# Kernel tuning notes

Measured on AMD Instinct MI355X. Metric: run time of the kernel, lower is better.

Reference implementation:

```python
import jax, jax.numpy as jnp
import numpy as np

NUM_BASES = 8
DEGREE = 3
KSIZE = 3
DOMAIN = (0.0, 1.0)


def bspline_basis(x, degree, knots):
    """Cox-de Boor recursion, vectorized over all elements of x.
    x: [...] float; knots: [num_bases + degree + 1].
    Returns basis values of shape [..., num_bases].
    (The original torch code evaluates this same recursion per-tap inside
    nested loops; here it is evaluated once, batched, with correct knot
    index bookkeeping. Uniform distinct knots -> no zero denominators.)
    """
    xe = x[..., None]  # [..., 1]
    # degree-0: indicator of each knot interval -> [..., L-1]
    B = ((knots[:-1] <= xe) & (xe < knots[1:])).astype(x.dtype)
    for d in range(1, degree + 1):
        left = (xe - knots[:-(d + 1)]) / (knots[d:-1] - knots[:-(d + 1)]) * B[..., :-1]
        right = (knots[d + 1:] - xe) / (knots[d + 1:] - knots[1:-d]) * B[..., 1:]
        B = left + right  # [..., L-d-1]
    return B  # [..., num_bases]


def setup_inputs() -> dict:
    key = jax.random.key(0)
    k1, k2 = jax.random.split(key)
    # inputs uniform in [0,1) so they lie inside the B-spline domain
    x = jax.random.uniform(k1, (16, 64, 64, 64), dtype=jnp.float32)
    # per-tap spline coefficients: [Cout, Cin, K, K, num_bases]
    coeff = jax.random.normal(k2, (64, 64, KSIZE, KSIZE, NUM_BASES), dtype=jnp.float32)
    return {"x": x, "coeff": coeff}


def reference(x, coeff):
    # normalize to domain (identity for domain=(0,1), kept for faithfulness)
    xn = (x - DOMAIN[0]) / (DOMAIN[1] - DOMAIN[0])
    knots = jnp.linspace(DOMAIN[0], DOMAIN[1], NUM_BASES + DEGREE + 1, dtype=x.dtype)
    # spline basis for every input element: [B, Cin, H, W, nb]
    phi = bspline_basis(xn, DEGREE, knots)
    Bn, Cin, H, W, nb = phi.shape
    Cout = coeff.shape[0]
    # The KAN conv  out[b,o,h,w] = sum_{j,k,l,m} phi[b,j,h+k,w+l,m]*coeff[o,j,k,l,m]
    # is exactly a VALID conv with Cin*nb input channels.
    phi_c = jnp.transpose(phi, (0, 1, 4, 2, 3)).reshape(Bn, Cin * nb, H, W)
    w = jnp.transpose(coeff, (0, 1, 4, 2, 3)).reshape(Cout, Cin * nb, KSIZE, KSIZE)
    out = jax.lax.conv_general_dilated(
        phi_c, w, window_strides=(1, 1), padding="VALID",
        dimension_numbers=("NCHW", "OIHW", "NCHW"))
    return out  # [B, Cout, H-K+1, W-K+1]
```

## Files before the change

kernel.cpp:

```cpp
#include <hip/hip_runtime.h>
#include <hip/hip_bf16.h>


typedef short v8s __attribute__((ext_vector_type(8)));
typedef float v4f __attribute__((ext_vector_type(4)));
typedef float v16f __attribute__((ext_vector_type(16)));
typedef unsigned long long u64;
typedef u64 v2u64 __attribute__((ext_vector_type(2)));

#define B_N   16
#define CIN   64
#define COUT  64
#define H_IN  64
#define W_IN  64
#define NB    8
#define HO    62
#define WO    62
#define JC    8
#define NCH   8

__device__ __forceinline__ ushort f2bf(float f) {
    uint xu = __float_as_uint(f);
    return (ushort)((xu + 0x7fffu + ((xu >> 16) & 1u)) >> 16);
}

__device__ __forceinline__ uint cvtpk(float a, float b) {
    uint r;
    asm("v_cvt_pk_bf16_f32 %0, %1, %2" : "=v"(r) : "v"(a), "v"(b));
    return r;
}

__global__ void prep_coeff_kernel(const float* __restrict__ coeff, ushort* __restrict__ bt) {
    int n = blockIdx.x * 256 + threadIdx.x;
    if (n >= 294912) return;
    int m  = n & 7;
    int g2 = (n >> 3) & 1;
    int o  = (n >> 4) & 63;
    int jp = (n >> 10) & 3;
    int q  = n >> 12;
    int tap = q % 9;
    int jc  = q / 9;
    int j = jc * 8 + jp * 2 + g2;
    bt[n] = f2bf(coeff[((o * CIN + j) * 9 + tap) * 8 + m]);
}

#define MFMA32(a, b, c) __builtin_amdgcn_mfma_f32_32x32x16_bf16((a), (b), (c), 0, 0, 0)
#define MFMA16(a, b, c) __builtin_amdgcn_mfma_f32_16x16x32_bf16((a), (b), (c), 0, 0, 0)

__global__ __launch_bounds__(512, 4) void kan_conv_hp2(
        const float* __restrict__ x, const ushort* __restrict__ cb,
        float* __restrict__ out) {
    extern __shared__ __align__(16) char smraw[];
    const int h0   = blockIdx.x * 2;
    const int b    = blockIdx.y;
    const int tid  = threadIdx.x;
    const int lane = tid & 63;
    const int wv   = tid >> 6;
    const int kh   = wv & 3;
    const int hh   = wv >> 2;
    const int l31  = lane & 31;
    const int g2   = lane >> 5;

    char* wrB = smraw + wv * 6144 + lane * 16;
    const char* rdB = smraw + wv * 6144 + g2 * 1024 + l31 * 16;

    v16f acc[2][2];
    acc[0][0] = (v16f)(0.f); acc[0][1] = (v16f)(0.f);
    acc[1][0] = (v16f)(0.f); acc[1][1] = (v16f)(0.f);

    float xr0[6], xr1[6];
    const float* xb = x + ((size_t)(b * CIN) * H_IN + (h0 + hh)) * W_IN + lane;
    const int jx = kh * 2;

#define XL(dst, jcn) { \
    _Pragma("unroll") \
    for (int e = 0; e < 6; ++e) \
        dst[e] = xb[(size_t)((jcn) * 8 + jx + (e & 1)) * (H_IN * W_IN) + (e >> 1) * W_IN]; \
    }

    auto PW = [&](float xval, int e) {
        float s_ = fminf(fmaxf(xval * 11.0f, 0.0f), 10.999f);
        int i0 = (int)s_;
        float u  = s_ - (float)i0;
        float um = 1.0f - u;
        float u2 = u * u, u3 = u2 * u;
        const float inv6 = 1.0f / 6.0f;
        float n0 = um * um * um * inv6;
        float n1 = (3.0f * u3 - 6.0f * u2 + 4.0f) * inv6;
        float n2 = (-3.0f * u3 + 3.0f * u2 + 3.0f * u + 1.0f) * inv6;
        float n3 = u3 * inv6;
        u64 V = (u64)cvtpk(n0, n1) | ((u64)cvtpk(n2, n3) << 32);
        int bi = i0 - 3;
        u64 lo = bi < 0 ? (V >> (uint)(-16 * bi))
               : bi < 4 ? (V << (uint)(16 * bi)) : 0ull;
        u64 hi = bi <= 0 ? 0ull
               : bi < 4 ? (V >> (uint)(64 - 16 * bi))
               : (V << (uint)(16 * bi - 64));
        v2u64 pk; pk[0] = lo; pk[1] = hi;
        *reinterpret_cast<v2u64*>(wrB + e * 1024) = pk;
    };
    auto TAP = [&](const char* pAc, int k, int lt, int tap) {
        v8s b0 = *reinterpret_cast<const v8s*>(rdB + k * 2048 + lt * 16);
        v8s b1 = *reinterpret_cast<const v8s*>(rdB + k * 2048 + 512 + lt * 16);
        v8s a0 = *reinterpret_cast<const v8s*>(pAc + tap * 8192);
        v8s a1 = *reinterpret_cast<const v8s*>(pAc + tap * 8192 + 1024);
        acc[0][0] = MFMA32(a0, b0, acc[0][0]);
        acc[0][1] = MFMA32(a0, b1, acc[0][1]);
        acc[1][0] = MFMA32(a1, b0, acc[1][0]);
        acc[1][1] = MFMA32(a1, b1, acc[1][1]);
    };

    const char* pA = (const char*)cb + (size_t)(kh * 128 + l31 * 2 + g2) * 16;

    XL(xr0, 0);
    PW(xr0[0], 0); PW(xr0[1], 1); PW(xr0[2], 2);
    PW(xr0[3], 3); PW(xr0[4], 4); PW(xr0[5], 5);
    XL(xr1, 1);

#define CHUNK(jc, CUR, NXT) { \
    const char* pAc = pA + (size_t)(jc) * 73728; \
    if ((jc) + 2 < NCH) XL(NXT, (jc) + 2); \
    TAP(pAc, 0, 0, 0); TAP(pAc, 0, 1, 1); TAP(pAc, 0, 2, 2); \
    if ((jc) + 1 < NCH) { PW(CUR[0], 0); PW(CUR[1], 1); } \
    TAP(pAc, 1, 0, 3); TAP(pAc, 1, 1, 4); TAP(pAc, 1, 2, 5); \
    if ((jc) + 1 < NCH) { PW(CUR[2], 2); PW(CUR[3], 3); } \
    TAP(pAc, 2, 0, 6); TAP(pAc, 2, 1, 7); TAP(pAc, 2, 2, 8); \
    if ((jc) + 1 < NCH) { PW(CUR[4], 4); PW(CUR[5], 5); } \
    }

    for (int jj = 0; jj < 4; ++jj) {
        CHUNK(2 * jj,     xr1, xr0);
        CHUNK(2 * jj + 1, xr0, xr1);
    }

#define WR_FULL(off) { \
    _Pragma("unroll") \
    for (int t = 0; t < 4; ++t) { \
        _Pragma("unroll") \
        for (int q = 0; q < 4; ++q) { \
            v4f v; \
            _Pragma("unroll") \
            for (int z = 0; z < 4; ++z) v[z] = acc[t >> 1][t & 1][q * 4 + z]; \
            *reinterpret_cast<v4f*>(smraw + (off) + (t * 4 + q) * 1024 + lane * 16) = v; \
        } } }
#define ADD_FULL(off) { \
    _Pragma("unroll") \
    for (int t = 0; t < 4; ++t) { \
        _Pragma("unroll") \
        for (int q = 0; q < 4; ++q) { \
            v4f v = *reinterpret_cast<const v4f*>(smraw + (off) + (t * 4 + q) * 1024 + lane * 16); \
            _Pragma("unroll") \
            for (int z = 0; z < 4; ++z) acc[t >> 1][t & 1][q * 4 + z] += v[z]; \
        } } }
#define WR_HALF(OT, off) { \
    _Pragma("unroll") \
    for (int wf = 0; wf < 2; ++wf) { \
        _Pragma("unroll") \
        for (int q = 0; q < 4; ++q) { \
            v4f v; \
            _Pragma("unroll") \
            for (int z = 0; z < 4; ++z) v[z] = acc[OT][wf][q * 4 + z]; \
            *reinterpret_cast<v4f*>(smraw + (off) + (wf * 4 + q) * 1024 + lane * 16) = v; \
        } } }
#define ADD_HALF(OT, off) { \
    _Pragma("unroll") \
    for (int wf = 0; wf < 2; ++wf) { \
        _Pragma("unroll") \
        for (int q = 0; q < 4; ++q) { \
            v4f v = *reinterpret_cast<const v4f*>(smraw + (off) + (wf * 4 + q) * 1024 + lane * 16); \
            _Pragma("unroll") \
            for (int z = 0; z < 4; ++z) acc[OT][wf][q * 4 + z] += v[z]; \
        } } }
#define STORE_HALF(OT) { \
    _Pragma("unroll") \
    for (int wf = 0; wf < 2; ++wf) { \
        int w = wf * 32 + l31; \
        if (w < WO) { \
            _Pragma("unroll") \
            for (int reg = 0; reg < 16; ++reg) { \
                int o = (OT) * 32 + (reg & 3) + 8 * (reg >> 2) + 4 * g2; \
                out[((b * COUT + o) * HO + (h0 + hh)) * WO + w] = acc[OT][wf][reg]; \
            } } } }

    const int ro = hh * 32768;
    __syncthreads();
    if (kh == 1) WR_FULL(ro);
    if (kh == 3) WR_FULL(ro + 16384);
    __syncthreads();
    if (kh == 0) ADD_FULL(ro);
    if (kh == 2) ADD_FULL(ro + 16384);
    __syncthreads();
    if (kh == 2) WR_HALF(0, ro);
    if (kh == 0) WR_HALF(1, ro + 8192);
    __syncthreads();
    if (kh == 0) { ADD_HALF(0, ro);        STORE_HALF(0); }
    if (kh == 2) { ADD_HALF(1, ro + 8192); STORE_HALF(1); }
}

__global__ __launch_bounds__(256, 4) void kan_conv_fb(
        const float* __restrict__ x, const float* __restrict__ coeff_f,
        float* __restrict__ out) {
    const int h    = blockIdx.x;
    const int b    = blockIdx.y;
    const int tid  = threadIdx.x;
    const int lane = tid & 63;
    const int wv   = tid >> 6;
    const int g    = lane >> 4;
    const int l15  = lane & 15;
    const int obase = (wv >> 1) << 5;
    const int wbase = (wv & 1) << 5;

    __shared__ __align__(16) ushort phi_lds[3 * JC * W_IN * NB];
    __shared__ uint lut[72];
    if (tid < 72) {
        int tap = tid;
        int j  = tap / 9;
        int r9 = tap - j * 9;
        int kt = r9 / 3;
        int lt = r9 - kt * 3;
        lut[tap] = (uint)(((kt * JC + j) * W_IN) * NB) | ((uint)lt << 16)
                 | ((uint)j << 20) | ((uint)r9 << 24);
    }
    v4f acc00 = {0.f, 0.f, 0.f, 0.f};
    v4f acc01 = acc00, acc10 = acc00, acc11 = acc00;
    const int aoff = obase + l15;
    float xv[6];
    #pragma unroll
    for (int it = 0; it < 6; ++it) {
        int n = it * 256 + tid;
        xv[it] = x[((b * CIN + ((n >> 6) & 7)) * H_IN + (h + (n >> 9))) * W_IN + (n & 63)];
    }
    for (int jc = 0; jc < NCH; ++jc) {
        #pragma unroll
        for (int it = 0; it < 6; ++it) {
            int n = it * 256 + tid;
            float s  = xv[it] * 11.0f;
            int i0 = (int)s;
            i0 = i0 < 0 ? 0 : (i0 > 10 ? 10 : i0);
            float u  = s - (float)i0;
            float um = 1.0f - u;
            float u2 = u * u, u3 = u2 * u;
            const float inv6 = 1.0f / 6.0f;
            float n0 = um * um * um * inv6;
            float n1 = (3.0f * u3 - 6.0f * u2 + 4.0f) * inv6;
            float n2 = (-3.0f * u3 + 3.0f * u2 + 3.0f * u + 1.0f) * inv6;
            float n3 = u3 * inv6;
            u64 V = (u64)f2bf(n0) | ((u64)f2bf(n1) << 16)
                  | ((u64)f2bf(n2) << 32) | ((u64)f2bf(n3) << 48);
            int bi = i0 - 3;
            u64 lo = bi < 0 ? (V >> (uint)(-16 * bi))
                   : bi < 4 ? (V << (uint)(16 * bi)) : 0ull;
            u64 hi = bi <= 0 ? 0ull
                   : bi < 4 ? (V >> (uint)(64 - 16 * bi))
                   : (V << (uint)(16 * bi - 64));
            v2u64 pk; pk[0] = lo; pk[1] = hi;
            *reinterpret_cast<v2u64*>(&phi_lds[n << 3]) = pk;
        }
        if (jc + 1 < NCH) {
            int j0n = (jc + 1) * JC;
            #pragma unroll
            for (int it = 0; it < 6; ++it) {
                int n = it * 256 + tid;
                xv[it] = x[((b * CIN + j0n + ((n >> 6) & 7)) * H_IN + (h + (n >> 9))) * W_IN + (n & 63)];
            }
        }
        __syncthreads();
        const int j0 = jc * JC;
        #pragma unroll 6
        for (int kk = 0; kk < 18; ++kk) {
            int tap = (kk << 2) + g;
            uint e = lut[tap];
            int philoc = (int)(e & 0xffffu);
            int lt     = (int)((e >> 16) & 3u);
            int w0 = wbase + l15 + lt;
            int w1 = w0 + 16;
            w0 = w0 < 63 ? w0 : 63;
            w1 = w1 < 63 ? w1 : 63;
            v8s pb0 = *reinterpret_cast<const v8s*>(&phi_lds[philoc + (w0 << 3)]);
            v8s pb1 = *reinterpret_cast<const v8s*>(&phi_lds[philoc + (w1 << 3)]);
            int j  = (int)((e >> 20) & 15u);
            int r9 = (int)((e >> 24) & 15u);
            const float* cf = coeff_f + (((aoff * CIN + (j0 + j)) * 9 + r9) << 3);
            v8s pa0, pa1;
            #pragma unroll
            for (int z = 0; z < 8; ++z) pa0[z] = (short)f2bf(cf[z]);
            const float* cf2 = cf + (CIN * 9 * NB * 16);
            #pragma unroll
            for (int z = 0; z < 8; ++z) pa1[z] = (short)f2bf(cf2[z]);
            acc00 = MFMA16(pa0, pb0, acc00);
            acc01 = MFMA16(pa0, pb1, acc01);
            acc10 = MFMA16(pa1, pb0, acc10);
            acc11 = MFMA16(pa1, pb1, acc11);
        }
        __syncthreads();
    }
    const int wc0 = wbase + l15;
    const int wc1 = wc0 + 16;
    #pragma unroll
    for (int i = 0; i < 2; ++i) {
        v4f a0 = (i == 0) ? acc00 : acc10;
        v4f a1 = (i == 0) ? acc01 : acc11;
        int o = obase + i * 16 + (g << 2);
        #pragma unroll
        for (int r = 0; r < 4; ++r) {
            int off = ((b * COUT + o + r) * HO + h) * WO;
            if (wc0 < WO) out[off + wc0] = a0[r];
            if (wc1 < WO) out[off + wc1] = a1[r];
        }
    }
}

extern "C" void kernel_launch(void* const* d_in, const int* in_sizes, int n_in,
                              void* d_out, int out_size, void* d_ws, size_t ws_size,
                              hipStream_t stream) {
    const float* x     = (const float*)d_in[0];
    const float* coeff = (const float*)d_in[1];
    float* out = (float*)d_out;

    const size_t bt_bytes = (size_t)294912 * 2;
    if (ws_size >= bt_bytes) {
        ushort* bt = (ushort*)d_ws;
        prep_coeff_kernel<<<(294912 + 255) / 256, 256, 0, stream>>>(coeff, bt);
        kan_conv_hp2<<<dim3(HO / 2, B_N), 512, 65536, stream>>>(x, bt, out);
    } else {
        kan_conv_fb<<<dim3(HO, B_N), 256, 0, stream>>>(x, coeff, out);
    }
}
```

Measured before the change: 53.88 us.

## Split waves by width halves and share basis rows across two output rows

Before, the two wave groups each handled one output row over the full width. Now each group handles half of the width for both output rows, and each wave stages 4 input rows of basis values so one B fragment feeds two adjacent output rows. LDS use per block drops from 64 KB to 34 KB, and the cross-wave reduction is rebuilt as a longer sequence of pair-wise write/add steps with extra barriers. The cubic basis weights also use fewer operations, with n2 taken from partition of unity. In exchange only 34 of 64 lanes stage inputs, there are more sync points, and the bf16 values shift slightly.

```diff
diff --git a/kernel.cpp b/kernel.cpp
--- a/kernel.cpp
+++ b/kernel.cpp
@@ -47,7 +47,7 @@
 #define MFMA32(a, b, c) __builtin_amdgcn_mfma_f32_32x32x16_bf16((a), (b), (c), 0, 0, 0)
 #define MFMA16(a, b, c) __builtin_amdgcn_mfma_f32_16x16x32_bf16((a), (b), (c), 0, 0, 0)
 
-__global__ __launch_bounds__(512, 4) void kan_conv_hp2(
+__global__ __launch_bounds__(512, 4) void kan_conv_hw(
         const float* __restrict__ x, const ushort* __restrict__ cb,
         float* __restrict__ out) {
     extern __shared__ __align__(16) char smraw[];
@@ -57,24 +57,26 @@
     const int lane = tid & 63;
     const int wv   = tid >> 6;
     const int kh   = wv & 3;
-    const int hh   = wv >> 2;
+    const int wh   = wv >> 2;
     const int l31  = lane & 31;
     const int g2   = lane >> 5;
 
-    char* wrB = smraw + wv * 6144 + lane * 16;
-    const char* rdB = smraw + wv * 6144 + g2 * 1024 + l31 * 16;
-
-    v16f acc[2][2];
-    acc[0][0] = (v16f)(0.f); acc[0][1] = (v16f)(0.f);
-    acc[1][0] = (v16f)(0.f); acc[1][1] = (v16f)(0.f);
-
-    float xr0[6], xr1[6];
-    const float* xb = x + ((size_t)(b * CIN) * H_IN + (h0 + hh)) * W_IN + lane;
-    const int jx = kh * 2;
-
-#define XL(dst, jcn) { \
-    _Pragma("unroll") \
-    for (int e = 0; e < 6; ++e) \
+    char* const regB = smraw + wv * 4352;
+    char* const wrB  = regB + lane * 16;
+    const char* const rdB = regB + g2 * 544 + l31 * 16;
+    const bool stg = lane < 34;
+
+    v16f c00 = (v16f)(0.f), c01 = (v16f)(0.f);
+    v16f c10 = (v16f)(0.f), c11 = (v16f)(0.f);
+
+    float xr0[8], xr1[8];
+    const int jx   = kh * 2;
+    const int wcol = min(wh * 32 + lane, 63);
+    const float* xb = x + ((size_t)(b * CIN) * H_IN + h0) * W_IN + wcol;
+
+#define XL(dst, jcn) if (stg) { \
+    _Pragma("unroll") \
+    for (int e = 0; e < 8; ++e) \
         dst[e] = xb[(size_t)((jcn) * 8 + jx + (e & 1)) * (H_IN * W_IN) + (e >> 1) * W_IN]; \
     }
 
@@ -82,13 +84,14 @@
         float s_ = fminf(fmaxf(xval * 11.0f, 0.0f), 10.999f);
         int i0 = (int)s_;
         float u  = s_ - (float)i0;
-        float um = 1.0f - u;
+        float t  = 1.0f - u;
         float u2 = u * u, u3 = u2 * u;
+        float t3 = t * t * t;
         const float inv6 = 1.0f / 6.0f;
-        float n0 = um * um * um * inv6;
-        float n1 = (3.0f * u3 - 6.0f * u2 + 4.0f) * inv6;
-        float n2 = (-3.0f * u3 + 3.0f * u2 + 3.0f * u + 1.0f) * inv6;
+        float n0 = t3 * inv6;
         float n3 = u3 * inv6;
+        float n1 = fmaf(u2, fmaf(u, 0.5f, -1.0f), 2.0f / 3.0f);
+        float n2 = 1.0f - n0 - n1 - n3;
         u64 V = (u64)cvtpk(n0, n1) | ((u64)cvtpk(n2, n3) << 32);
         int bi = i0 - 3;
         u64 lo = bi < 0 ? (V >> (uint)(-16 * bi))
@@ -96,25 +99,27 @@
         u64 hi = bi <= 0 ? 0ull
                : bi < 4 ? (V >> (uint)(64 - 16 * bi))
                : (V << (uint)(16 * bi - 64));
-        v2u64 pk; pk[0] = lo; pk[1] = hi;
-        *reinterpret_cast<v2u64*>(wrB + e * 1024) = pk;
+        if (stg) {
+            v2u64 pk; pk[0] = lo; pk[1] = hi;
+            *reinterpret_cast<v2u64*>(wrB + e * 544) = pk;
+        }
     };
     auto TAP = [&](const char* pAc, int k, int lt, int tap) {
-        v8s b0 = *reinterpret_cast<const v8s*>(rdB + k * 2048 + lt * 16);
-        v8s b1 = *reinterpret_cast<const v8s*>(rdB + k * 2048 + 512 + lt * 16);
-        v8s a0 = *reinterpret_cast<const v8s*>(pAc + tap * 8192);
-        v8s a1 = *reinterpret_cast<const v8s*>(pAc + tap * 8192 + 1024);
-        acc[0][0] = MFMA32(a0, b0, acc[0][0]);
-        acc[0][1] = MFMA32(a0, b1, acc[0][1]);
-        acc[1][0] = MFMA32(a1, b0, acc[1][0]);
-        acc[1][1] = MFMA32(a1, b1, acc[1][1]);
+        v8s bh0 = *reinterpret_cast<const v8s*>(rdB + k * 1088 + lt * 16);
+        v8s bh1 = *reinterpret_cast<const v8s*>(rdB + (k + 1) * 1088 + lt * 16);
+        v8s a0  = *reinterpret_cast<const v8s*>(pAc + tap * 8192);
+        v8s a1  = *reinterpret_cast<const v8s*>(pAc + tap * 8192 + 1024);
+        c00 = MFMA32(a0, bh0, c00);
+        c01 = MFMA32(a1, bh0, c01);
+        c10 = MFMA32(a0, bh1, c10);
+        c11 = MFMA32(a1, bh1, c11);
     };
 
     const char* pA = (const char*)cb + (size_t)(kh * 128 + l31 * 2 + g2) * 16;
 
     XL(xr0, 0);
-    PW(xr0[0], 0); PW(xr0[1], 1); PW(xr0[2], 2);
-    PW(xr0[3], 3); PW(xr0[4], 4); PW(xr0[5], 5);
+    PW(xr0[0], 0); PW(xr0[1], 1); PW(xr0[2], 2); PW(xr0[3], 3);
+    PW(xr0[4], 4); PW(xr0[5], 5); PW(xr0[6], 6); PW(xr0[7], 7);
     XL(xr1, 1);
 
 #define CHUNK(jc, CUR, NXT) { \
@@ -125,7 +130,7 @@
     TAP(pAc, 1, 0, 3); TAP(pAc, 1, 1, 4); TAP(pAc, 1, 2, 5); \
     if ((jc) + 1 < NCH) { PW(CUR[2], 2); PW(CUR[3], 3); } \
     TAP(pAc, 2, 0, 6); TAP(pAc, 2, 1, 7); TAP(pAc, 2, 2, 8); \
-    if ((jc) + 1 < NCH) { PW(CUR[4], 4); PW(CUR[5], 5); } \
+    if ((jc) + 1 < NCH) { PW(CUR[4], 4); PW(CUR[5], 5); PW(CUR[6], 6); PW(CUR[7], 7); } \
     }
 
     for (int jj = 0; jj < 4; ++jj) {
@@ -133,68 +138,62 @@
         CHUNK(2 * jj + 1, xr0, xr1);
     }
 
-#define WR_FULL(off) { \
-    _Pragma("unroll") \
-    for (int t = 0; t < 4; ++t) { \
-        _Pragma("unroll") \
-        for (int q = 0; q < 4; ++q) { \
-            v4f v; \
-            _Pragma("unroll") \
-            for (int z = 0; z < 4; ++z) v[z] = acc[t >> 1][t & 1][q * 4 + z]; \
-            *reinterpret_cast<v4f*>(smraw + (off) + (t * 4 + q) * 1024 + lane * 16) = v; \
+#define WR_PAIR(CA, CB, off) { \
+    _Pragma("unroll") \
+    for (int q = 0; q < 4; ++q) { \
+        v4f v; \
+        _Pragma("unroll") \
+        for (int z = 0; z < 4; ++z) v[z] = CA[q * 4 + z]; \
+        *reinterpret_cast<v4f*>(smraw + (off) + q * 1024 + lane * 16) = v; \
+    } \
+    _Pragma("unroll") \
+    for (int q = 0; q < 4; ++q) { \
+        v4f v; \
+        _Pragma("unroll") \
+        for (int z = 0; z < 4; ++z) v[z] = CB[q * 4 + z]; \
+        *reinterpret_cast<v4f*>(smraw + (off) + 4096 + q * 1024 + lane * 16) = v; \
+    } }
+#define ADD_PAIR(CA, CB, off) { \
+    _Pragma("unroll") \
+    for (int q = 0; q < 4; ++q) { \
+        v4f v = *reinterpret_cast<const v4f*>(smraw + (off) + q * 1024 + lane * 16); \
+        _Pragma("unroll") \
+        for (int z = 0; z < 4; ++z) CA[q * 4 + z] += v[z]; \
+    } \
+    _Pragma("unroll") \
+    for (int q = 0; q < 4; ++q) { \
+        v4f v = *reinterpret_cast<const v4f*>(smraw + (off) + 4096 + q * 1024 + lane * 16); \
+        _Pragma("unroll") \
+        for (int z = 0; z < 4; ++z) CB[q * 4 + z] += v[z]; \
+    } }
+#define STORE_PAIR(CA, CB, H) { \
+    int w = wh * 32 + l31; \
+    if (w < WO) { \
+        _Pragma("unroll") \
+        for (int reg = 0; reg < 16; ++reg) { \
+            int o = (reg & 3) + 8 * (reg >> 2) + 4 * g2; \
+            out[((b * COUT + o) * HO + (h0 + (H))) * WO + w] = CA[reg]; \
+            out[((b * COUT + o + 32) * HO + (h0 + (H))) * WO + w] = CB[reg]; \
         } } }
-#define ADD_FULL(off) { \
-    _Pragma("unroll") \
-    for (int t = 0; t < 4; ++t) { \
-        _Pragma("unroll") \
-        for (int q = 0; q < 4; ++q) { \
-            v4f v = *reinterpret_cast<const v4f*>(smraw + (off) + (t * 4 + q) * 1024 + lane * 16); \
-            _Pragma("unroll") \
-            for (int z = 0; z < 4; ++z) acc[t >> 1][t & 1][q * 4 + z] += v[z]; \
-        } } }
-#define WR_HALF(OT, off) { \
-    _Pragma("unroll") \
-    for (int wf = 0; wf < 2; ++wf) { \
-        _Pragma("unroll") \
-        for (int q = 0; q < 4; ++q) { \
-            v4f v; \
-            _Pragma("unroll") \
-            for (int z = 0; z < 4; ++z) v[z] = acc[OT][wf][q * 4 + z]; \
-            *reinterpret_cast<v4f*>(smraw + (off) + (wf * 4 + q) * 1024 + lane * 16) = v; \
-        } } }
-#define ADD_HALF(OT, off) { \
-    _Pragma("unroll") \
-    for (int wf = 0; wf < 2; ++wf) { \
-        _Pragma("unroll") \
-        for (int q = 0; q < 4; ++q) { \
-            v4f v = *reinterpret_cast<const v4f*>(smraw + (off) + (wf * 4 + q) * 1024 + lane * 16); \
-            _Pragma("unroll") \
-            for (int z = 0; z < 4; ++z) acc[OT][wf][q * 4 + z] += v[z]; \
-        } } }
-#define STORE_HALF(OT) { \
-    _Pragma("unroll") \
-    for (int wf = 0; wf < 2; ++wf) { \
-        int w = wf * 32 + l31; \
-        if (w < WO) { \
-            _Pragma("unroll") \
-            for (int reg = 0; reg < 16; ++reg) { \
-                int o = (OT) * 32 + (reg & 3) + 8 * (reg >> 2) + 4 * g2; \
-                out[((b * COUT + o) * HO + (h0 + hh)) * WO + w] = acc[OT][wf][reg]; \
-            } } } }
-
-    const int ro = hh * 32768;
-    __syncthreads();
-    if (kh == 1) WR_FULL(ro);
-    if (kh == 3) WR_FULL(ro + 16384);
-    __syncthreads();
-    if (kh == 0) ADD_FULL(ro);
-    if (kh == 2) ADD_FULL(ro + 16384);
-    __syncthreads();
-    if (kh == 2) WR_HALF(0, ro);
-    if (kh == 0) WR_HALF(1, ro + 8192);
-    __syncthreads();
-    if (kh == 0) { ADD_HALF(0, ro);        STORE_HALF(0); }
-    if (kh == 2) { ADD_HALF(1, ro + 8192); STORE_HALF(1); }
+
+    __syncthreads();
+    if (kh == 1) WR_PAIR(c00, c01, wh * 8192);
+    if (kh == 3) WR_PAIR(c00, c01, 16384 + wh * 8192);
+    __syncthreads();
+    if (kh == 0) ADD_PAIR(c00, c01, wh * 8192);
+    if (kh == 2) ADD_PAIR(c00, c01, 16384 + wh * 8192);
+    __syncthreads();
+    if (kh == 1) WR_PAIR(c10, c11, wh * 8192);
+    if (kh == 3) WR_PAIR(c10, c11, 16384 + wh * 8192);
+    __syncthreads();
+    if (kh == 0) ADD_PAIR(c10, c11, wh * 8192);
+    if (kh == 2) ADD_PAIR(c10, c11, 16384 + wh * 8192);
+    __syncthreads();
+    if (kh == 2) WR_PAIR(c00, c01, wh * 8192);
+    if (kh == 0) WR_PAIR(c10, c11, 16384 + wh * 8192);
+    __syncthreads();
+    if (kh == 0) { ADD_PAIR(c00, c01, wh * 8192);         STORE_PAIR(c00, c01, 0); }
+    if (kh == 2) { ADD_PAIR(c10, c11, 16384 + wh * 8192); STORE_PAIR(c10, c11, 1); }
 }
 
 __global__ __launch_bounds__(256, 4) void kan_conv_fb(
@@ -321,7 +320,7 @@
     if (ws_size >= bt_bytes) {
         ushort* bt = (ushort*)d_ws;
         prep_coeff_kernel<<<(294912 + 255) / 256, 256, 0, stream>>>(coeff, bt);
-        kan_conv_hp2<<<dim3(HO / 2, B_N), 512, 65536, stream>>>(x, bt, out);
+        kan_conv_hw<<<dim3(HO / 2, B_N), 512, 34816, stream>>>(x, bt, out);
     } else {
         kan_conv_fb<<<dim3(HO, B_N), 256, 0, stream>>>(x, coeff, out);
     }
```

Result: slower. 55.29 us (+2.6%).
